# Kernel optimization log

Hardware: AMD Instinct MI355X
Metric: run time of the kernel (lower is better)

Reference implementation:

```python
import jax, jax.numpy as jnp
import numpy as np

N = 10000   # nodes
E = 32768   # edges
IN = 6      # input node feature dim
H = 64      # hidden_channels
OUT = 3     # out_channels (edge types)
EA = 4      # edge attribute dim


def setup_inputs() -> dict:
    key = jax.random.key(0)
    ks = jax.random.split(key, 20)
    rn = lambda k, shape, s=0.05: (jax.random.normal(k, shape, jnp.float32) * s)
    inp = {
        "x": jax.random.normal(ks[0], (N, IN), jnp.float32),
        "edge_index": jax.random.randint(ks[1], (2, E), 0, N, jnp.int64),
        "edge_attributes": jax.random.uniform(ks[2], (E, EA), jnp.float32),
        # edge_nn1: Linear(4, 6*H) -> ReLU -> Linear(6*H, 6*H); produces conv1 per-edge weight [IN, H]
        "e1w1": rn(ks[3], (EA, IN * H)),
        "e1b1": jnp.zeros((IN * H,), jnp.float32),
        "e1w2": rn(ks[4], (IN * H, IN * H)),
        "e1b2": jnp.zeros((IN * H,), jnp.float32),
        "root1": rn(ks[5], (IN, H)),
        "bias1": jnp.zeros((H,), jnp.float32),
        # edge_nn2: Linear(4, H*H) -> ReLU -> Linear(H*H, H*H); produces conv2 per-edge weight [H, H]
        "e2w1": rn(ks[6], (EA, H * H), 0.02),
        "e2b1": jnp.zeros((H * H,), jnp.float32),
        "e2w2": rn(ks[7], (H * H, H * H), 0.02),
        "e2b2": jnp.zeros((H * H,), jnp.float32),
        "root2": rn(ks[8], (H, H)),
        "bias2": jnp.zeros((H,), jnp.float32),
        # fc_edge: Linear(2*H + 4, OUT)
        "fcw": rn(ks[9], (2 * H + EA, OUT)),
        "fcb": jnp.zeros((OUT,), jnp.float32),
    }
    return inp


def _nnconv(x, edge_attr, src, dst, w1, b1, w2, b2, root, bias, in_c, out_c):
    # edge MLP -> per-edge weight matrix [E, in_c, out_c]
    w = jax.nn.relu(edge_attr @ w1 + b1) @ w2 + b2
    w = w.reshape(-1, in_c, out_c)
    # gather src features, batched per-edge matmul
    msg = jnp.einsum("ei,eio->eo", x[src], w)  # [E, out_c]
    n = x.shape[0]
    s = jax.ops.segment_sum(msg, dst, num_segments=n)
    cnt = jax.ops.segment_sum(jnp.ones((msg.shape[0], 1), msg.dtype), dst, num_segments=n)
    agg = s / jnp.maximum(cnt, 1.0)  # scatter-mean; isolated nodes stay 0
    return agg + x @ root + bias


def reference(x, edge_index, edge_attributes,
              e1w1, e1b1, e1w2, e1b2, root1, bias1,
              e2w1, e2b1, e2w2, e2b2, root2, bias2,
              fcw, fcb):
    src, dst = edge_index[0], edge_index[1]
    h = jax.nn.relu(_nnconv(x, edge_attributes, src, dst, e1w1, e1b1, e1w2, e1b2, root1, bias1, IN, H))
    h = jax.nn.relu(_nnconv(h, edge_attributes, src, dst, e2w1, e2b1, e2w2, e2b2, root2, bias2, H, H))
    hs, hd = h[src], h[dst]
    edge_prob = jax.nn.sigmoid(jnp.sum(hs * hd, axis=1, keepdims=True))  # [E, 1]
    combined = jnp.concatenate([hs, hd, edge_attributes], axis=1)  # [E, 2H+4]
    edge_types = jax.nn.softmax(combined @ fcw + fcb, axis=1)  # [E, 3]
    return edge_prob, edge_types, src, dst
```

## Files before the change

kernel.cpp:

```cpp
#include <hip/hip_runtime.h>

#define N_NODES 10000
#define E_EDGES 32768
#define NEB (E_EDGES/64)

typedef short bf16x8v __attribute__((ext_vector_type(8)));
typedef short bf16x4v __attribute__((ext_vector_type(4)));
typedef float f32x4   __attribute__((ext_vector_type(4)));
typedef float f32x2   __attribute__((ext_vector_type(2)));

__device__ __forceinline__ float bf2f(ushort u){
    union{ uint i; float f; } v; v.i = ((uint)u) << 16; return v.f;
}
__device__ __forceinline__ ushort f2bf(float f){
    union{ float f; uint i; } v; v.f = f;
    uint u = v.i;
    return (ushort)((u + 0x7fffu + ((u >> 16) & 1u)) >> 16);
}
__device__ __forceinline__ float ldf(float v){ return v; }
__device__ __forceinline__ float ldf(ushort v){ return bf2f(v); }

__device__ __forceinline__ f32x2 pk_fma(f32x2 a, f32x2 b, f32x2 c){
    f32x2 d;
    asm("v_pk_fma_f32 %0, %1, %2, %3" : "=v"(d) : "v"(a), "v"(b), "v"(c));
    return d;
}

__device__ __forceinline__ void async_copy16(const void* g, void* l){
    __builtin_amdgcn_global_load_lds(
        (const __attribute__((address_space(1))) void*)g,
        (__attribute__((address_space(3))) void*)l, 16, 0, 0);
}
__device__ __forceinline__ void wait_vm0(){ __builtin_amdgcn_s_waitcnt(0x0F70); }

__global__ void idx_detect(const int* __restrict__ w, int* __restrict__ flag){
    __shared__ int sh[256];
    int t = threadIdx.x;
    int o = 0;
    for (int i = 2*t + 1; i < 2*E_EDGES; i += 512) o |= w[i];
    sh[t] = o; __syncthreads();
    for (int s = 128; s; s >>= 1){ if (t < s) sh[t] |= sh[t+s]; __syncthreads(); }
    if (t == 0) *flag = sh[0];
}

__global__ void idx_norm(const int* __restrict__ w, const int* __restrict__ flag,
                         int* __restrict__ srcN, int* __restrict__ dstN){
    int e = blockIdx.x*256 + threadIdx.x;
    if (e >= E_EDGES) return;
    int s, d;
    if (*flag){ s = w[e];     d = w[E_EDGES + e]; }
    else      { s = w[2*e];   d = w[2*E_EDGES + 2*e]; }
    s = min(max(s, 0), N_NODES-1);
    d = min(max(d, 0), N_NODES-1);
    srcN[e] = s; dstN[e] = d;
}

template<int K, int NI, int KS, typename TH>
__global__ __launch_bounds__(256, 2)
void gemm_msg(const float* __restrict__ ea4,
              const int* __restrict__ srcI, const int* __restrict__ dstI,
              const float* __restrict__ w1, const float* __restrict__ b1,
              const ushort* __restrict__ Bt, const float* __restrict__ b2,
              const TH* __restrict__ hsrc,
              float* __restrict__ nodesum)
{
    constexpr int CH = K / 64 / KS;
    constexpr int IP = NI / 2;
    constexpr int NT = IP * CH;

    __shared__ __align__(16) ushort pool[16512];
    __shared__ __align__(16) ushort h_s[NI][68];
    __shared__ float ea_s[256];
    __shared__ int src_s[64];
    __shared__ int dst_s[64];

    const int bid  = blockIdx.x;
    const int eb   = bid % NEB;
    const int kz   = bid / NEB;
    const int t    = threadIdx.x;
    const int e0   = eb * 64;
    const int lane = t & 63;
    const int wv   = t >> 6;
    const int ng   = wv & 1;
    const int kg   = wv >> 1;
    const int q    = lane >> 4;
    const int ln   = lane & 15;

    if (t < 64){ src_s[t] = srcI[e0 + t]; dst_s[t] = dstI[e0 + t]; }
    ea_s[t] = ea4[e0 * 4 + t];
    __syncthreads();

    if (NI == 64){
        int r = t >> 2, ig = t & 3;
        const ushort* hp = (const ushort*)hsrc + (size_t)src_s[r] * 64 + ig * 16;
        uint4 v0 = *(const uint4*)(hp);
        uint4 v1 = *(const uint4*)(hp + 8);
        const ushort* p0 = (const ushort*)&v0;
        const ushort* p1 = (const ushort*)&v1;
        #pragma unroll
        for (int ii = 0; ii < 8; ii++) h_s[ig*16 + ii    ][r] = p0[ii];
        #pragma unroll
        for (int ii = 0; ii < 8; ii++) h_s[ig*16 + 8 + ii][r] = p1[ii];
    } else {
        if (t < 64){
            const TH* hp = hsrc + (size_t)src_s[t] * NI;
            #pragma unroll
            for (int ii = 0; ii < NI; ii++) h_s[ii][t] = f2bf(ldf(hp[ii]));
        }
    }

    #pragma unroll 1
    for (int kc = 0; kc < CH; kc++){
        int kcg = kz * CH + kc;
        #pragma unroll
        for (int s2 = 0; s2 < 2; s2++){
            int a = t + s2 * 256;
            int r = a >> 3, oct = a & 7;
            int k = kcg * 64 + oct * 8;
            f32x2 a2[4];
            float4 b0 = *(const float4*)(b1 + k);
            float4 b4 = *(const float4*)(b1 + k + 4);
            a2[0] = f32x2{b0.x, b0.y}; a2[1] = f32x2{b0.z, b0.w};
            a2[2] = f32x2{b4.x, b4.y}; a2[3] = f32x2{b4.z, b4.w};
            #pragma unroll
            for (int a4 = 0; a4 < 4; a4++){
                float4 w0 = *(const float4*)(w1 + (size_t)a4 * K + k);
                float4 w4 = *(const float4*)(w1 + (size_t)a4 * K + k + 4);
                float m = ea_s[r * 4 + a4];
                f32x2 mm = {m, m};
                a2[0] = pk_fma(mm, f32x2{w0.x, w0.y}, a2[0]);
                a2[1] = pk_fma(mm, f32x2{w0.z, w0.w}, a2[1]);
                a2[2] = pk_fma(mm, f32x2{w4.x, w4.y}, a2[2]);
                a2[3] = pk_fma(mm, f32x2{w4.z, w4.w}, a2[3]);
            }
            uint4 ov;
            ushort* po = (ushort*)&ov;
            #pragma unroll
            for (int j = 0; j < 8; j++) po[j] = f2bf(fmaxf(a2[j >> 1][j & 1], 0.f));
            *(uint4*)&pool[kc * 4096 + r * 64 + ((oct ^ (r & 7)) * 8)] = ov;
        }
    }
    __syncthreads();

    const int j0 = kg * 4 + q;
    bf16x8v afA[CH][4];
    #pragma unroll
    for (int kc = 0; kc < CH; kc++)
        #pragma unroll
        for (int ms = 0; ms < 4; ms++){
            int r = ms * 16 + ln;
            afA[kc][ms] = *(const bf16x8v*)&pool[kc * 4096 + r * 64 + ((j0 ^ (r & 7)) * 8)];
        }
    __syncthreads();

    const int rl4 = lane >> 2;
    const int ocp = (lane & 3) ^ ((lane >> 3) & 3);
    ushort* const lb0 = &pool[(wv * 2 + 0) * 2048];
    ushort* const lb1 = &pool[(wv * 2 + 1) * 2048];
    auto laneAddr = [&](int ip, int kc) -> const ushort* {
        return Bt + (size_t)(ip * 128 + ng * 64 + rl4) * K
                  + (size_t)(kz * CH + kc) * 64 + kg * 32 + ocp * 8;
    };
    auto issue = [&](const ushort* ga, ushort* lbase){
        #pragma unroll
        for (int j = 0; j < 4; j++)
            async_copy16(ga + (size_t)j * 16 * K, lbase + j * 512);
    };

    issue(laneAddr(0, 0), lb0);

    const ushort* gp1 = laneAddr(0, 1);
    int kcn = 1;
    constexpr size_t STRIDE_WRAP = (size_t)128 * K - (size_t)(CH - 1) * 64;

    f32x2 msgp[4][4][2];
    #pragma unroll
    for (int a = 0; a < 4; a++)
        #pragma unroll
        for (int b = 0; b < 4; b++){
            msgp[a][b][0] = f32x2{0.f, 0.f};
            msgp[a][b][1] = f32x2{0.f, 0.f};
        }

    const f32x4 fzero = {0.f, 0.f, 0.f, 0.f};
    const int bslot = (ln * 4 + (q ^ ((ln >> 1) & 3))) * 8;
    int g = 0;
    #pragma unroll 1
    for (int ip = 0; ip < IP; ip++){
        f32x4 acc[4][4];
        #pragma unroll
        for (int kc = 0; kc < CH; kc++, g++){
            ushort* const bcur = ((kc & 1) == 0) ? lb0 : lb1;
            ushort* const bnxt = ((kc & 1) == 0) ? lb1 : lb0;

            wait_vm0();
            __builtin_amdgcn_sched_barrier(0);

            if (g + 1 < NT){
                issue(gp1, bnxt);
                gp1 += (kcn == CH - 1) ? STRIDE_WRAP : (size_t)64;
                kcn  = (kcn == CH - 1) ? 0 : kcn + 1;
            }

            bf16x8v bfr[4];
            #pragma unroll
            for (int ns = 0; ns < 4; ns++)
                bfr[ns] = *(const bf16x8v*)&bcur[ns * 512 + bslot];

            __builtin_amdgcn_s_setprio(1);
            #pragma unroll
            for (int ms = 0; ms < 4; ms++)
                #pragma unroll
                for (int ns = 0; ns < 4; ns++)
                    acc[ms][ns] = __builtin_amdgcn_mfma_f32_16x16x32_bf16(
                        afA[kc][ms], bfr[ns], (kc == 0) ? fzero : acc[ms][ns], 0, 0, 0);
            __builtin_amdgcn_s_setprio(0);
        }
        int i2 = ip * 2 + ng;
        #pragma unroll
        for (int ms = 0; ms < 4; ms++){
            bf16x4v hb = *(const bf16x4v*)&h_s[i2][ms * 16 + q * 4];
            f32x2 h01, h23;
            h01[0] = bf2f((ushort)hb[0]); h01[1] = bf2f((ushort)hb[1]);
            h23[0] = bf2f((ushort)hb[2]); h23[1] = bf2f((ushort)hb[3]);
            #pragma unroll
            for (int ns = 0; ns < 4; ns++){
                f32x2 lo = __builtin_shufflevector(acc[ms][ns], acc[ms][ns], 0, 1);
                f32x2 hi = __builtin_shufflevector(acc[ms][ns], acc[ms][ns], 2, 3);
                msgp[ms][ns][0] = pk_fma(h01, lo, msgp[ms][ns][0]);
                msgp[ms][ns][1] = pk_fma(h23, hi, msgp[ms][ns][1]);
            }
        }
    }

    __syncthreads();
    float* mr  = (float*)&pool[0];
    float* b2s = (float*)&pool[0] + 4160;
    if (kz == 0){
        for (int i = t; i < NI * 64; i += 256) b2s[i] = b2[i];
    }
    #pragma unroll 1
    for (int r4 = 0; r4 < 4; r4++){
        if (wv == r4){
            #pragma unroll
            for (int ms = 0; ms < 4; ms++)
                #pragma unroll
                for (int ns = 0; ns < 4; ns++)
                    #pragma unroll
                    for (int j = 0; j < 4; j++){
                        int row = ms * 16 + q * 4 + j, col = ns * 16 + ln;
                        float v = msgp[ms][ns][j >> 1][j & 1];
                        if (r4 == 0) mr[row * 65 + col]  = v;
                        else         mr[row * 65 + col] += v;
                    }
        }
        __syncthreads();
    }
    #pragma unroll 1
    for (int s2 = 0; s2 < 16; s2++){
        int a = t + s2 * 256;
        int row = a >> 6, o = a & 63;
        float v = mr[row * 65 + o];
        if (kz == 0){
            #pragma unroll 4
            for (int ii = 0; ii < NI; ii++)
                v += bf2f(h_s[ii][row]) * b2s[ii * 64 + o];
        }
        atomicAdd(nodesum + (size_t)dst_s[row] * 64 + o, v);
    }
}

__global__ void transpose_f2b(const float* __restrict__ in, ushort* __restrict__ out, int D){
    __shared__ float tl[32][33];
    int bx = blockIdx.x, by = blockIdx.y;
    int tx = threadIdx.x, ty = threadIdx.y;
    #pragma unroll
    for (int r = 0; r < 4; r++)
        tl[ty + 8*r][tx] = in[(size_t)(by*32 + ty + 8*r) * D + bx*32 + tx];
    __syncthreads();
    #pragma unroll
    for (int r = 0; r < 4; r++)
        out[(size_t)(bx*32 + ty + 8*r) * D + by*32 + tx] = f2bf(tl[tx][ty + 8*r]);
}

__global__ void count_k(const int* __restrict__ dstI, float* __restrict__ cnt){
    int e = blockIdx.x * 256 + threadIdx.x;
    if (e < E_EDGES) atomicAdd(cnt + dstI[e], 1.f);
}

template<int NIn, typename TI>
__global__ void node_k(const float* __restrict__ ns_, const float* __restrict__ cnt,
                       const TI* __restrict__ xin, const float* __restrict__ root,
                       const float* __restrict__ bias,
                       ushort* __restrict__ hb, float* __restrict__ hf, int Nn)
{
    int idx = blockIdx.x * 256 + threadIdx.x;
    if (idx >= Nn * 64) return;
    int n = idx >> 6, o = idx & 63;
    float c = cnt[n];
    float inv = c > 1.f ? 1.f / c : 1.f;
    float s = ns_[idx] * inv + bias[o];
    #pragma unroll
    for (int i = 0; i < NIn; i++)
        s += ldf(xin[(size_t)n * NIn + i]) * root[i * 64 + o];
    s = fmaxf(s, 0.f);
    if (hb) hb[idx] = f2bf(s);
    else    hf[idx] = s;
}

__global__ void edge_out_k(const float* __restrict__ h2, const int* __restrict__ srcI,
                           const int* __restrict__ dstI, const float* __restrict__ ea,
                           const float* __restrict__ fcw, const float* __restrict__ fcb,
                           float* __restrict__ out)
{
    __shared__ float fw[396];
    __shared__ float fb[3];
    int t = threadIdx.x;
    for (int i = t; i < 396; i += 256) fw[i] = fcw[i];
    if (t < 3) fb[t] = fcb[t];
    __syncthreads();
    int e = blockIdx.x * 256 + t;
    int s = srcI[e], d = dstI[e];
    const float* hs = h2 + (size_t)s * 64;
    const float* hd = h2 + (size_t)d * 64;
    float dot = 0.f, l0 = fb[0], l1 = fb[1], l2 = fb[2];
    #pragma unroll 8
    for (int c = 0; c < 64; c++){
        float a = hs[c], b = hd[c];
        dot += a * b;
        l0 += a * fw[c*3+0] + b * fw[(64+c)*3+0];
        l1 += a * fw[c*3+1] + b * fw[(64+c)*3+1];
        l2 += a * fw[c*3+2] + b * fw[(64+c)*3+2];
    }
    #pragma unroll
    for (int a4 = 0; a4 < 4; a4++){
        float v = ea[e*4 + a4];
        l0 += v * fw[(128+a4)*3+0];
        l1 += v * fw[(128+a4)*3+1];
        l2 += v * fw[(128+a4)*3+2];
    }
    float prob = 1.f / (1.f + __expf(-dot));
    float m  = fmaxf(l0, fmaxf(l1, l2));
    float x0 = __expf(l0 - m), x1 = __expf(l1 - m), x2 = __expf(l2 - m);
    float inv = 1.f / (x0 + x1 + x2);
    out[e]                  = prob;
    out[E_EDGES + 3*e + 0]  = x0 * inv;
    out[E_EDGES + 3*e + 1]  = x1 * inv;
    out[E_EDGES + 3*e + 2]  = x2 * inv;
    out[4*E_EDGES + e]      = (float)s;
    out[5*E_EDGES + e]      = (float)d;
}

extern "C" void kernel_launch(void* const* d_in, const int* in_sizes, int n_in,
                              void* d_out, int out_size, void* d_ws, size_t ws_size,
                              hipStream_t stream)
{
    const float* x     = (const float*)d_in[0];
    const int*   ei    = (const int*)  d_in[1];
    const float* ea    = (const float*)d_in[2];
    const float* e1w1  = (const float*)d_in[3];
    const float* e1b1  = (const float*)d_in[4];
    const float* e1w2  = (const float*)d_in[5];
    const float* e1b2  = (const float*)d_in[6];
    const float* root1 = (const float*)d_in[7];
    const float* bias1 = (const float*)d_in[8];
    const float* e2w1  = (const float*)d_in[9];
    const float* e2b1  = (const float*)d_in[10];
    const float* e2w2  = (const float*)d_in[11];
    const float* e2b2  = (const float*)d_in[12];
    const float* root2 = (const float*)d_in[13];
    const float* bias2 = (const float*)d_in[14];
    const float* fcw   = (const float*)d_in[15];
    const float* fcb   = (const float*)d_in[16];

    char* ws = (char*)d_ws;
    float*  ns1  = (float*) (ws + 0);
    float*  ns2  = (float*) (ws + 2560000);
    float*  cnt  = (float*) (ws + 5120000);
    int*    flag = (int*)   (ws + 5160000);
    int*    srcN = (int*)   (ws + 5160064);
    int*    dstN = (int*)   (ws + 5291136);
    ushort* h1   = (ushort*)(ws + 5422208);
    float*  h2   = (float*) (ws + 6702208);
    ushort* B1t  = (ushort*)(ws + 9262208);
    ushort* B2t  = (ushort*)(ws + 9557120);

    hipMemsetAsync(d_ws, 0, 5160064, stream);

    idx_detect<<<1, 256, 0, stream>>>(ei, flag);
    idx_norm<<<128, 256, 0, stream>>>(ei, flag, srcN, dstN);

    transpose_f2b<<<dim3(12, 12),  dim3(32, 8), 0, stream>>>(e1w2, B1t, 384);
    transpose_f2b<<<dim3(128,128), dim3(32, 8), 0, stream>>>(e2w2, B2t, 4096);
    count_k<<<128, 256, 0, stream>>>(dstN, cnt);

    gemm_msg<384, 6, 3, float><<<NEB*3, 256, 0, stream>>>(ea, srcN, dstN, e1w1, e1b1, B1t, e1b2, x, ns1);
    node_k<6, float><<<2500, 256, 0, stream>>>(ns1, cnt, x, root1, bias1, h1, nullptr, N_NODES);

    gemm_msg<4096, 64, 16, ushort><<<NEB*16, 256, 0, stream>>>(ea, srcN, dstN, e2w1, e2b1, B2t, e2b2, h1, ns2);
    node_k<64, ushort><<<2500, 256, 0, stream>>>(ns2, cnt, h1, root2, bias2, nullptr, h2, N_NODES);

    edge_out_k<<<128, 256, 0, stream>>>(h2, srcN, dstN, ea, fcw, fcb, (float*)d_out);
}
```

Baseline: 1.540 ms.

## Prepack B weights into MFMA fragment order and load directly to registers

Replaces the plain transpose of the second-layer edge-MLP weights with a pack kernel that writes bf16 tiles already arranged in MFMA B-fragment order. The GEMM then reads B fragments straight from global memory into registers with fully coalesced 16-byte loads, double-buffered in registers (bA/bB), instead of using async global-to-LDS copies with waitcnt and LDS reads. This removes the LDS staging and its synchronisation, but relies on caches and register prefetch to hide global latency. The pack kernel's reads are strided across rows, so it may coalesce poorly.

```diff
diff --git a/kernel.cpp b/kernel.cpp
--- a/kernel.cpp
+++ b/kernel.cpp
@@ -25,13 +25,6 @@
     asm("v_pk_fma_f32 %0, %1, %2, %3" : "=v"(d) : "v"(a), "v"(b), "v"(c));
     return d;
 }
-
-__device__ __forceinline__ void async_copy16(const void* g, void* l){
-    __builtin_amdgcn_global_load_lds(
-        (const __attribute__((address_space(1))) void*)g,
-        (__attribute__((address_space(3))) void*)l, 16, 0, 0);
-}
-__device__ __forceinline__ void wait_vm0(){ __builtin_amdgcn_s_waitcnt(0x0F70); }
 
 __global__ void idx_detect(const int* __restrict__ w, int* __restrict__ flag){
     __shared__ int sh[256];
@@ -53,6 +46,32 @@
     s = min(max(s, 0), N_NODES-1);
     d = min(max(d, 0), N_NODES-1);
     srcN[e] = s; dstN[e] = d;
+}
+
+template<int K, int IP, int CH>
+__global__ void pack_b(const float* __restrict__ w2, ushort* __restrict__ out){
+    constexpr int ROWS = IP * 128;
+    const int kcg = blockIdx.x;
+    const int rs  = blockIdx.y;
+    const int t   = threadIdx.x;
+    const int ip  = rs >> 1, ng = rs & 1;
+    const int kz  = kcg / CH, kc = kcg % CH;
+    #pragma unroll
+    for (int h = 0; h < 2; h++){
+        int u512 = t + h * 256;
+        int kg   = u512 >> 8;
+        int u    = u512 & 255;
+        int ns   = u >> 6, lane = u & 63;
+        int q    = lane >> 4, ln = lane & 15;
+        int row   = ip * 128 + ng * 64 + ns * 16 + ln;
+        int kbase = kcg * 64 + kg * 32 + q * 8;
+        size_t tile = ((size_t)(kz * IP + ip) * CH + kc) * 4 + (kg * 2 + ng);
+        ushort vv[8];
+        #pragma unroll
+        for (int j = 0; j < 8; j++)
+            vv[j] = f2bf(w2[(size_t)(kbase + j) * ROWS + row]);
+        *(uint4*)&out[tile * 2048 + (size_t)u * 8] = *(const uint4*)vv;
+    }
 }
 
 template<int K, int NI, int KS, typename TH>
@@ -66,7 +85,6 @@
 {
     constexpr int CH = K / 64 / KS;
     constexpr int IP = NI / 2;
-    constexpr int NT = IP * CH;
 
     __shared__ __align__(16) ushort pool[16512];
     __shared__ __align__(16) ushort h_s[NI][68];
@@ -153,25 +171,7 @@
         }
     __syncthreads();
 
-    const int rl4 = lane >> 2;
-    const int ocp = (lane & 3) ^ ((lane >> 3) & 3);
-    ushort* const lb0 = &pool[(wv * 2 + 0) * 2048];
-    ushort* const lb1 = &pool[(wv * 2 + 1) * 2048];
-    auto laneAddr = [&](int ip, int kc) -> const ushort* {
-        return Bt + (size_t)(ip * 128 + ng * 64 + rl4) * K
-                  + (size_t)(kz * CH + kc) * 64 + kg * 32 + ocp * 8;
-    };
-    auto issue = [&](const ushort* ga, ushort* lbase){
-        #pragma unroll
-        for (int j = 0; j < 4; j++)
-            async_copy16(ga + (size_t)j * 16 * K, lbase + j * 512);
-    };
-
-    issue(laneAddr(0, 0), lb0);
-
-    const ushort* gp1 = laneAddr(0, 1);
-    int kcn = 1;
-    constexpr size_t STRIDE_WRAP = (size_t)128 * K - (size_t)(CH - 1) * 64;
+    const ushort* gp0 = Bt + ((size_t)(kz * IP * CH) * 4 + wv) * 2048 + lane * 8;
 
     f32x2 msgp[4][4][2];
     #pragma unroll
@@ -183,29 +183,22 @@
         }
 
     const f32x4 fzero = {0.f, 0.f, 0.f, 0.f};
-    const int bslot = (ln * 4 + (q ^ ((ln >> 1) & 3))) * 8;
-    int g = 0;
+
+    bf16x8v bA[4], bB[4];
+    #pragma unroll
+    for (int ns = 0; ns < 4; ns++)
+        bA[ns] = *(const bf16x8v*)(gp0 + ns * 512);
+    gp0 += 8192;
+
     #pragma unroll 1
     for (int ip = 0; ip < IP; ip++){
         f32x4 acc[4][4];
         #pragma unroll
-        for (int kc = 0; kc < CH; kc++, g++){
-            ushort* const bcur = ((kc & 1) == 0) ? lb0 : lb1;
-            ushort* const bnxt = ((kc & 1) == 0) ? lb1 : lb0;
-
-            wait_vm0();
-            __builtin_amdgcn_sched_barrier(0);
-
-            if (g + 1 < NT){
-                issue(gp1, bnxt);
-                gp1 += (kcn == CH - 1) ? STRIDE_WRAP : (size_t)64;
-                kcn  = (kcn == CH - 1) ? 0 : kcn + 1;
-            }
-
-            bf16x8v bfr[4];
+        for (int kc = 0; kc < CH; kc += 2){
             #pragma unroll
             for (int ns = 0; ns < 4; ns++)
-                bfr[ns] = *(const bf16x8v*)&bcur[ns * 512 + bslot];
+                bB[ns] = *(const bf16x8v*)(gp0 + ns * 512);
+            gp0 += 8192;
 
             __builtin_amdgcn_s_setprio(1);
             #pragma unroll
@@ -213,7 +206,23 @@
                 #pragma unroll
                 for (int ns = 0; ns < 4; ns++)
                     acc[ms][ns] = __builtin_amdgcn_mfma_f32_16x16x32_bf16(
-                        afA[kc][ms], bfr[ns], (kc == 0) ? fzero : acc[ms][ns], 0, 0, 0);
+                        afA[kc][ms], bA[ns], (kc == 0) ? fzero : acc[ms][ns], 0, 0, 0);
+            __builtin_amdgcn_s_setprio(0);
+
+            if (kc + 2 < CH || ip < IP - 1){
+                #pragma unroll
+                for (int ns = 0; ns < 4; ns++)
+                    bA[ns] = *(const bf16x8v*)(gp0 + ns * 512);
+                gp0 += 8192;
+            }
+
+            __builtin_amdgcn_s_setprio(1);
+            #pragma unroll
+            for (int ms = 0; ms < 4; ms++)
+                #pragma unroll
+                for (int ns = 0; ns < 4; ns++)
+                    acc[ms][ns] = __builtin_amdgcn_mfma_f32_16x16x32_bf16(
+                        afA[kc + 1][ms], bB[ns], acc[ms][ns], 0, 0, 0);
             __builtin_amdgcn_s_setprio(0);
         }
         int i2 = ip * 2 + ng;
@@ -268,19 +277,6 @@
         }
         atomicAdd(nodesum + (size_t)dst_s[row] * 64 + o, v);
     }
-}
-
-__global__ void transpose_f2b(const float* __restrict__ in, ushort* __restrict__ out, int D){
-    __shared__ float tl[32][33];
-    int bx = blockIdx.x, by = blockIdx.y;
-    int tx = threadIdx.x, ty = threadIdx.y;
-    #pragma unroll
-    for (int r = 0; r < 4; r++)
-        tl[ty + 8*r][tx] = in[(size_t)(by*32 + ty + 8*r) * D + bx*32 + tx];
-    __syncthreads();
-    #pragma unroll
-    for (int r = 0; r < 4; r++)
-        out[(size_t)(bx*32 + ty + 8*r) * D + by*32 + tx] = f2bf(tl[tx][ty + 8*r]);
 }
 
 __global__ void count_k(const int* __restrict__ dstI, float* __restrict__ cnt){
@@ -390,8 +386,8 @@
     idx_detect<<<1, 256, 0, stream>>>(ei, flag);
     idx_norm<<<128, 256, 0, stream>>>(ei, flag, srcN, dstN);
 
-    transpose_f2b<<<dim3(12, 12),  dim3(32, 8), 0, stream>>>(e1w2, B1t, 384);
-    transpose_f2b<<<dim3(128,128), dim3(32, 8), 0, stream>>>(e2w2, B2t, 4096);
+    pack_b<384, 3, 2><<<dim3(6, 6), 256, 0, stream>>>(e1w2, B1t);
+    pack_b<4096, 32, 4><<<dim3(64, 64), 256, 0, stream>>>(e2w2, B2t);
     count_k<<<128, 256, 0, stream>>>(dstN, cnt);
 
     gemm_msg<384, 6, 3, float><<<NEB*3, 256, 0, stream>>>(ea, srcN, dstN, e1w1, e1b1, B1t, e1b2, x, ns1);
```

Result: faster. 1.242 ms (median of 2 runs) (-19.4%).
